# Kernel tuning notes

Hardware: AMD Instinct MI355X
Metric: run time of the kernel (lower is better)

## Reference

```python
import jax, jax.numpy as jnp
import numpy as np

NUM_GRAPHS = 128
NODES_PER_GRAPH = 512
NUM_NODES = NUM_GRAPHS * NODES_PER_GRAPH
NUM_EDGES = NUM_NODES * 16
IN_DIM = 64
HID = 128
NUM_HEADS = 4
BN_EPS = 1e-5


def setup_inputs() -> dict:
    key = jax.random.key(0)
    ks = jax.random.split(key, 12)
    x = jax.random.normal(ks[0], (NUM_NODES, IN_DIM), dtype=jnp.float32)
    edge_index = jax.random.randint(ks[1], (2, NUM_EDGES), 0, NUM_NODES, dtype=jnp.int32)
    batch = jnp.repeat(jnp.arange(NUM_GRAPHS, dtype=jnp.int32), NODES_PER_GRAPH)
    s = 0.05
    W0 = jax.random.normal(ks[2], (IN_DIM, HID), dtype=jnp.float32) * s
    b0 = jnp.zeros((HID,), jnp.float32)
    Wh = jax.random.normal(ks[3], (3, HID, HID), dtype=jnp.float32) * s  # convs 1..3
    bh = jnp.zeros((3, HID), jnp.float32)
    bn_gamma = jnp.ones((4, HID), jnp.float32)
    bn_beta = jnp.zeros((4, HID), jnp.float32)
    bn_mean = jnp.zeros((4, HID), jnp.float32)
    bn_var = jnp.ones((4, HID), jnp.float32)
    attn_in_w = jax.random.normal(ks[4], (3 * HID, HID), dtype=jnp.float32) * s
    attn_in_b = jnp.zeros((3 * HID,), jnp.float32)
    attn_out_w = jax.random.normal(ks[5], (HID, HID), dtype=jnp.float32) * s
    attn_out_b = jnp.zeros((HID,), jnp.float32)
    return dict(x=x, W0=W0, b0=b0, Wh=Wh, bh=bh, bn_gamma=bn_gamma, bn_beta=bn_beta,
                bn_mean=bn_mean, bn_var=bn_var, attn_in_w=attn_in_w, attn_in_b=attn_in_b,
                attn_out_w=attn_out_w, attn_out_b=attn_out_b, edge_index=edge_index, batch=batch)


def _forward(x, W0, b0, Wh, bh, bn_gamma, bn_beta, bn_mean, bn_var,
             attn_in_w, attn_in_b, attn_out_w, attn_out_b, edge_index, batch):
    N = x.shape[0]
    src, dst = edge_index[0], edge_index[1]
    # GCN symmetric normalization with self-loops (PyG GCNConv)
    deg = jax.ops.segment_sum(jnp.ones_like(src, jnp.float32), dst, num_segments=N) + 1.0
    dis = jax.lax.rsqrt(deg)                      # deg^{-1/2}
    enorm = (dis[src] * dis[dst])[:, None]        # per-edge norm
    self_norm = (dis * dis)[:, None]              # self-loop norm

    def gcn(h, W, b):
        h = h @ W
        agg = jax.ops.segment_sum(h[src] * enorm, dst, num_segments=N)
        return agg + h * self_norm + b

    def bn(h, i):
        scale = bn_gamma[i] * jax.lax.rsqrt(bn_var[i] + BN_EPS)
        return (h - bn_mean[i]) * scale + bn_beta[i]  # eval-mode BN

    # dropout is identity in eval mode
    h = jax.nn.relu(bn(gcn(x, W0, b0), 0))
    h = jax.nn.relu(bn(gcn(h, Wh[0], bh[0]), 1))
    h = jax.nn.relu(bn(gcn(h, Wh[1], bh[1]), 2))
    f = jax.nn.relu(bn(gcn(h, Wh[2], bh[2]), 3))   # [N, HID]

    # per-graph self-attention (equal-size contiguous graphs -> batched MHA)
    dh = HID // NUM_HEADS
    xg = f.reshape(NUM_GRAPHS, NODES_PER_GRAPH, HID)
    qkv = xg @ attn_in_w.T + attn_in_b            # [G, n, 3H]
    q, k, v = jnp.split(qkv, 3, axis=-1)

    def heads(t):
        return t.reshape(NUM_GRAPHS, NODES_PER_GRAPH, NUM_HEADS, dh).transpose(0, 2, 1, 3)
    q, k, v = heads(q), heads(k), heads(v)
    scores = jnp.einsum('ghnd,ghmd->ghnm', q, k) / np.sqrt(dh).astype(np.float32)
    attn = jax.nn.softmax(scores, axis=-1)
    o = jnp.einsum('ghnm,ghmd->ghnd', attn, v).transpose(0, 2, 1, 3).reshape(NUM_GRAPHS, NODES_PER_GRAPH, HID)
    o = o @ attn_out_w.T + attn_out_b
    final = o.reshape(N, HID)

    # global mean pool over batch indices
    cnt = jax.ops.segment_sum(jnp.ones((N,), jnp.float32), batch, num_segments=NUM_GRAPHS)
    graph_emb = jax.ops.segment_sum(final, batch, num_segments=NUM_GRAPHS) / cnt[:, None]
    return final, graph_emb


def reference(x, W0, b0, Wh, bh, bn_gamma, bn_beta, bn_mean, bn_var,
              attn_in_w, attn_in_b, attn_out_w, attn_out_b, edge_index, batch):
    return _forward(x, W0, b0, Wh, bh, bn_gamma, bn_beta, bn_mean, bn_var,
                    attn_in_w, attn_in_b, attn_out_w, attn_out_b, edge_index, batch)
```

## Files before the change

### kernel.cpp

```cpp
#include <hip/hip_runtime.h>
#include <hip/hip_bf16.h>
#include <cstdint>
#include <cstddef>

#define N_NODES 65536
#define N_EDGES 1048576
#define N_GRAPHS 128
#define NPG 512
#define IN_DIM 64
#define HID 128
#define BN_EPS 1e-5f

typedef __attribute__((ext_vector_type(8))) short bf16x8;
typedef __attribute__((ext_vector_type(4))) float f32x4;
typedef __attribute__((ext_vector_type(8))) unsigned short u16x8;

__device__ inline unsigned short f2bf(float f) {
  unsigned u = __builtin_bit_cast(unsigned, f);
  u = u + 0x7fffu + ((u >> 16) & 1u);
  return (unsigned short)(u >> 16);
}
__device__ inline float bf2f(unsigned short h) {
  unsigned u = ((unsigned)h) << 16;
  return __builtin_bit_cast(float, u);
}
__device__ inline void split_bf(float v, unsigned short& hi, unsigned short& lo) {
  hi = f2bf(v);
  lo = f2bf(v - bf2f(hi));
}
__device__ inline void split_bf_fast(float v, unsigned short& hi, unsigned short& lo) {
  unsigned u = __builtin_bit_cast(unsigned, v);
  hi = (unsigned short)(u >> 16);
  float r = v - __builtin_bit_cast(float, u & 0xffff0000u);
  lo = f2bf(r);
}

__global__ __launch_bounds__(256) void hist_kernel(const int* __restrict__ dst,
                                                   int* __restrict__ deg) {
  int e = blockIdx.x * 256 + threadIdx.x;
  if (e < N_EDGES) atomicAdd(&deg[dst[e]], 1);
}

__global__ __launch_bounds__(256) void dis_kernel(const int* __restrict__ deg,
                                                  float* __restrict__ dis) {
  int n = blockIdx.x * 256 + threadIdx.x;
  if (n < N_NODES) dis[n] = 1.0f / sqrtf((float)deg[n] + 1.0f);
}

__global__ __launch_bounds__(1024) void scan_kernel(const int* __restrict__ deg,
                                                    int* __restrict__ offsets,
                                                    int* __restrict__ cursor) {
  __shared__ int sums[1024];
  int t = threadIdx.x;
  int base = t * 64;
  const int4* dp = (const int4*)(deg + base);
  int s = 0;
#pragma unroll
  for (int i = 0; i < 16; i++) {
    int4 v = dp[i];
    s += v.x + v.y + v.z + v.w;
  }
  sums[t] = s;
  __syncthreads();
  for (int off = 1; off < 1024; off <<= 1) {
    int v = (t >= off) ? sums[t - off] : 0;
    __syncthreads();
    sums[t] += v;
    __syncthreads();
  }
  int run = (t == 0) ? 0 : sums[t - 1];
#pragma unroll
  for (int i = 0; i < 16; i++) {
    int4 v = dp[i];
    int idx = base + i * 4;
    offsets[idx] = run; cursor[idx] = run; run += v.x;
    offsets[idx + 1] = run; cursor[idx + 1] = run; run += v.y;
    offsets[idx + 2] = run; cursor[idx + 2] = run; run += v.z;
    offsets[idx + 3] = run; cursor[idx + 3] = run; run += v.w;
  }
  if (t == 1023) offsets[N_NODES] = run;
}

__global__ __launch_bounds__(256) void fill_kernel(const int* __restrict__ src,
                                                   const int* __restrict__ dst,
                                                   int* __restrict__ cursor,
                                                   int* __restrict__ csr) {
  int e = blockIdx.x * 256 + threadIdx.x;
  if (e < N_EDGES) {
    int d = dst[e];
    int slot = atomicAdd(&cursor[d], 1);
    csr[slot] = src[e];
  }
}

__global__ __launch_bounds__(256) void agg64_kernel(const float* __restrict__ x,
                                                    const float* __restrict__ dis,
                                                    const int* __restrict__ offsets,
                                                    const int* __restrict__ csr,
                                                    unsigned short* __restrict__ zhi,
                                                    unsigned short* __restrict__ zlo) {
  int node = blockIdx.x * 4 + (threadIdx.x >> 6);
  int lane = threadIdx.x & 63;
  float dn = dis[node];
  float acc = x[(size_t)node * 64 + lane] * dn * dn;
  int beg = offsets[node], end = offsets[node + 1];
  int k = beg;
  for (; k + 4 <= end; k += 4) {
    int s0 = csr[k], s1 = csr[k + 1], s2 = csr[k + 2], s3 = csr[k + 3];
    float w0 = dn * dis[s0], w1 = dn * dis[s1], w2 = dn * dis[s2], w3 = dn * dis[s3];
    float v0 = x[(size_t)s0 * 64 + lane];
    float v1 = x[(size_t)s1 * 64 + lane];
    float v2 = x[(size_t)s2 * 64 + lane];
    float v3 = x[(size_t)s3 * 64 + lane];
    acc = fmaf(w0, v0, acc);
    acc = fmaf(w1, v1, acc);
    acc = fmaf(w2, v2, acc);
    acc = fmaf(w3, v3, acc);
  }
  for (; k < end; k++) {
    int s = csr[k];
    acc = fmaf(dn * dis[s], x[(size_t)s * 64 + lane], acc);
  }
  unsigned short h_, l_;
  split_bf(acc, h_, l_);
  zhi[(size_t)node * 64 + lane] = h_;
  zlo[(size_t)node * 64 + lane] = l_;
}

__global__ __launch_bounds__(256) void agg128_kernel(const float* __restrict__ h,
                                                     const float* __restrict__ dis,
                                                     const int* __restrict__ offsets,
                                                     const int* __restrict__ csr,
                                                     unsigned short* __restrict__ zhi,
                                                     unsigned short* __restrict__ zlo) {
  int node = blockIdx.x * 4 + (threadIdx.x >> 6);
  int lane = threadIdx.x & 63;
  float dn = dis[node];
  float sn = dn * dn;
  const float* hr = h + (size_t)node * 128;
  float a0 = hr[lane] * sn;
  float a1 = hr[lane + 64] * sn;
  int beg = offsets[node], end = offsets[node + 1];
  int k = beg;
  for (; k + 4 <= end; k += 4) {
    int s0 = csr[k], s1 = csr[k + 1], s2 = csr[k + 2], s3 = csr[k + 3];
    float w0 = dn * dis[s0], w1 = dn * dis[s1], w2 = dn * dis[s2], w3 = dn * dis[s3];
    const float* p0 = h + (size_t)s0 * 128;
    const float* p1 = h + (size_t)s1 * 128;
    const float* p2 = h + (size_t)s2 * 128;
    const float* p3 = h + (size_t)s3 * 128;
    float u0 = p0[lane], d0 = p0[lane + 64];
    float u1 = p1[lane], d1 = p1[lane + 64];
    float u2 = p2[lane], d2 = p2[lane + 64];
    float u3 = p3[lane], d3 = p3[lane + 64];
    a0 = fmaf(w0, u0, a0); a1 = fmaf(w0, d0, a1);
    a0 = fmaf(w1, u1, a0); a1 = fmaf(w1, d1, a1);
    a0 = fmaf(w2, u2, a0); a1 = fmaf(w2, d2, a1);
    a0 = fmaf(w3, u3, a0); a1 = fmaf(w3, d3, a1);
  }
  for (; k < end; k++) {
    int s = csr[k];
    float w = dn * dis[s];
    const float* hs = h + (size_t)s * 128;
    a0 = fmaf(w, hs[lane], a0);
    a1 = fmaf(w, hs[lane + 64], a1);
  }
  unsigned short h0, l0, h1, l1;
  split_bf(a0, h0, l0);
  split_bf(a1, h1, l1);
  zhi[(size_t)node * 128 + lane] = h0;
  zlo[(size_t)node * 128 + lane] = l0;
  zhi[(size_t)node * 128 + lane + 64] = h1;
  zlo[(size_t)node * 128 + lane + 64] = l1;
}

template <bool TRANS>
__global__ __launch_bounds__(256) void wprep_kernel(const float* __restrict__ W, int K, int O,
                                                    unsigned short* __restrict__ hi,
                                                    unsigned short* __restrict__ lo) {
  int idx = blockIdx.x * 256 + threadIdx.x;
  int KC = K / 32;
  int total = (O / 16) * KC * 64;
  if (idx >= total) return;
  int lane = idx & 63;
  int rest = idx >> 6;
  int kc = rest % KC;
  int nt = rest / KC;
  int n = nt * 16 + (lane & 15);
  int kb = kc * 32 + (lane >> 4) * 8;
  unsigned short* hp = hi + (size_t)idx * 8;
  unsigned short* lp = lo + (size_t)idx * 8;
#pragma unroll
  for (int j = 0; j < 8; j++) {
    int k = kb + j;
    float v = TRANS ? W[(size_t)n * K + k] : W[(size_t)k * O + n];
    unsigned short h_, l_;
    split_bf(v, h_, l_);
    hp[j] = h_;
    lp[j] = l_;
  }
}

template <int K, int O, bool DOBN, bool DORELU, bool SPLIT_OUT, bool GROUPED,
          bool DOPOOL = false>
__global__ __launch_bounds__(256) void gemm_mfma(
    const unsigned short* __restrict__ Ahi, const unsigned short* __restrict__ Alo,
    const unsigned short* __restrict__ Whi, const unsigned short* __restrict__ Wlo,
    const float* __restrict__ bias,
    const float* __restrict__ gamma, const float* __restrict__ beta,
    const float* __restrict__ mean, const float* __restrict__ var,
    float* __restrict__ Cf, unsigned short* __restrict__ Chi,
    unsigned short* __restrict__ Clo, float* __restrict__ Pool = nullptr) {
  constexpr int KC = K / 32;
  int wave = threadIdx.x >> 6;
  int lane = threadIdx.x & 63;
  int m0 = blockIdx.x * 128 + wave * 32;
  int o0 = blockIdx.y * 128;
  int mrow = lane & 15;
  int kseg = (lane >> 4) * 8;

  f32x4 acc[2][8];
#pragma unroll
  for (int mt = 0; mt < 2; mt++)
#pragma unroll
    for (int nt = 0; nt < 8; nt++) acc[mt][nt] = (f32x4)0.0f;

#pragma unroll
  for (int kc = 0; kc < KC; kc++) {
    bf16x8 ah[2], al[2];
#pragma unroll
    for (int mt = 0; mt < 2; mt++) {
      size_t aoff = (size_t)(m0 + mt * 16 + mrow) * K + kc * 32 + kseg;
      ah[mt] = *(const bf16x8*)(Ahi + aoff);
      al[mt] = *(const bf16x8*)(Alo + aoff);
    }
#pragma unroll
    for (int nt = 0; nt < 8; nt++) {
      size_t foff = (((size_t)(blockIdx.y * 8 + nt) * KC + kc) * 64 + lane) * 8;
      bf16x8 bh = *(const bf16x8*)(Whi + foff);
      bf16x8 bl = *(const bf16x8*)(Wlo + foff);
#pragma unroll
      for (int mt = 0; mt < 2; mt++) {
        acc[mt][nt] = __builtin_amdgcn_mfma_f32_16x16x32_bf16(ah[mt], bh, acc[mt][nt], 0, 0, 0);
        acc[mt][nt] = __builtin_amdgcn_mfma_f32_16x16x32_bf16(ah[mt], bl, acc[mt][nt], 0, 0, 0);
        acc[mt][nt] = __builtin_amdgcn_mfma_f32_16x16x32_bf16(al[mt], bh, acc[mt][nt], 0, 0, 0);
        acc[mt][nt] = __builtin_amdgcn_mfma_f32_16x16x32_bf16(al[mt], bl, acc[mt][nt], 0, 0, 0);
      }
    }
  }

  int ccol = lane & 15;
  int crow0 = (lane >> 4) * 4;
  float colsum[8];
  if constexpr (DOPOOL) {
#pragma unroll
    for (int nt = 0; nt < 8; nt++) colsum[nt] = 0.0f;
  }
#pragma unroll
  for (int nt = 0; nt < 8; nt++) {
    int c = o0 + nt * 16 + ccol;
    float sc, cb;
    float b = bias[c];
    if (DOBN) {
      sc = gamma[c] * rsqrtf(var[c] + BN_EPS);
      cb = (b - mean[c]) * sc + beta[c];
    } else {
      sc = 1.0f;
      cb = b;
    }
#pragma unroll
    for (int mt = 0; mt < 2; mt++) {
#pragma unroll
      for (int r = 0; r < 4; r++) {
        float v = fmaf(acc[mt][nt][r], sc, cb);
        if (DORELU) v = fmaxf(v, 0.0f);
        size_t row = (size_t)(m0 + mt * 16 + crow0 + r);
        if (SPLIT_OUT) {
          unsigned short h_, l_;
          split_bf(v, h_, l_);
          if (GROUPED) {
            size_t base = row * (size_t)(2 * O) + (size_t)(((c >> 5) << 6) + (c & 31));
            Chi[base] = h_;
            Chi[base + 32] = l_;
          } else {
            Chi[row * O + c] = h_;
            Clo[row * O + c] = l_;
          }
        } else {
          Cf[row * O + c] = v;
        }
        if constexpr (DOPOOL) colsum[nt] += v;
      }
    }
  }
  if constexpr (DOPOOL) {
    __shared__ float pb[4][128];
#pragma unroll
    for (int nt = 0; nt < 8; nt++) {
      float cs = colsum[nt];
      cs += __shfl_xor(cs, 16, 64);
      cs += __shfl_xor(cs, 32, 64);
      if ((lane >> 4) == 0) pb[wave][nt * 16 + ccol] = cs;
    }
    __syncthreads();
    int tt = threadIdx.x;
    if (tt < 128) {
      float s2 = pb[0][tt] + pb[1][tt] + pb[2][tt] + pb[3][tt];
      int gg = blockIdx.x >> 2;
      atomicAdd(&Pool[gg * 128 + tt], s2 * (1.0f / NPG));
    }
  }
}

__global__ __launch_bounds__(256) void knorm_kernel(const unsigned short* __restrict__ qvs,
                                                    float* __restrict__ kmax2) {
  int g = blockIdx.x >> 2;
  int h = blockIdx.x & 3;
  size_t gbase = (size_t)g * NPG;
  float best = 0.0f;
#pragma unroll
  for (int r = 0; r < 2; r++) {
    int j = r * 256 + threadIdx.x;
    size_t base = (gbase + j) * 768 + (size_t)(4 + h) * 64;
    float s = 0.0f;
#pragma unroll
    for (int i = 0; i < 4; i++) {
      u16x8 hh = *(const u16x8*)(qvs + base + i * 8);
      u16x8 ll = *(const u16x8*)(qvs + base + 32 + i * 8);
#pragma unroll
      for (int jj = 0; jj < 8; jj++) {
        float v = bf2f(hh[jj]) + bf2f(ll[jj]);
        s = fmaf(v, v, s);
      }
    }
    best = fmaxf(best, s);
  }
#pragma unroll
  for (int off = 32; off >= 1; off >>= 1)
    best = fmaxf(best, __shfl_xor(best, off, 64));
  __shared__ float red[4];
  int wave = threadIdx.x >> 6;
  if ((threadIdx.x & 63) == 0) red[wave] = best;
  __syncthreads();
  if (threadIdx.x == 0) {
    float m = fmaxf(fmaxf(red[0], red[1]), fmaxf(red[2], red[3]));
    kmax2[blockIdx.x] = m;
  }
}

__global__ __launch_bounds__(256, 2) void attn_mfma_kernel(
    const unsigned short* __restrict__ qvs, const float* __restrict__ kmax2,
    unsigned short* __restrict__ ohi, unsigned short* __restrict__ olo) {
  int wb = ((blockIdx.x & 7) << 7) | (blockIdx.x >> 3);
  int g = wb >> 3;
  int h = (wb >> 1) & 3;
  int half = wb & 1;
  int t = threadIdx.x;
  int wave = t >> 6;
  int lane = t & 63;
  int quad = lane >> 4;
  int l15 = lane & 15;
  size_t gbase = (size_t)g * NPG;
  int qb = half * 256 + wave * 64;

  const float cf = 0.17677669529663687f * 1.4426950408889634f;

  __shared__ unsigned short Kh[2][32][40] __attribute__((aligned(16)));
  __shared__ unsigned short Kl[2][32][40] __attribute__((aligned(16)));
  __shared__ unsigned short Vh[2][33][40] __attribute__((aligned(16)));
  __shared__ unsigned short Vl[2][33][40] __attribute__((aligned(16)));
  __shared__ char wbuf[4][11264] __attribute__((aligned(16)));

  unsigned short* Ph = (unsigned short*)wbuf[wave];
  unsigned short* Pl = Ph + 64 * 44;
  float* Ot = (float*)wbuf[wave];

  bf16x8 qh[4], ql[4];
  float qn2p[4];
#pragma unroll
  for (int mt = 0; mt < 4; mt++) {
    size_t qoff = (gbase + qb + mt * 16 + l15) * 768 + (size_t)h * 64 + quad * 8;
    u16x8 hh = *(const u16x8*)(qvs + qoff);
    u16x8 ll = *(const u16x8*)(qvs + qoff + 32);
    qh[mt] = __builtin_bit_cast(bf16x8, hh);
    ql[mt] = __builtin_bit_cast(bf16x8, ll);
    float s = 0.0f;
#pragma unroll
    for (int j = 0; j < 8; j++) {
      float v = bf2f(hh[j]) + bf2f(ll[j]);
      s = fmaf(v, v, s);
    }
    s += __shfl_xor(s, 16);
    s += __shfl_xor(s, 32);
    qn2p[mt] = s;
  }
  if (quad == 0) {
#pragma unroll
    for (int mt = 0; mt < 4; mt++) Ot[mt * 16 + l15] = qn2p[mt];
  }
  float km2 = kmax2[g * 4 + h];
  float Mq[4][4];
#pragma unroll
  for (int mt = 0; mt < 4; mt++)
#pragma unroll
    for (int r = 0; r < 4; r++)
      Mq[mt][r] = cf * sqrtf(Ot[mt * 16 + quad * 4 + r] * km2);

  f32x4 Oa[4][3];
#pragma unroll
  for (int mt = 0; mt < 4; mt++)
#pragma unroll
    for (int nt = 0; nt < 3; nt++) Oa[mt][nt] = (f32x4)0.0f;

  if (t >= 64 && t < 72) {
    int u = t - 64;
    int bsel = u >> 2;
    int i = u & 3;
    u16x8 ones;
#pragma unroll
    for (int j = 0; j < 8; j++) ones[j] = 0x3F80;
    *(u16x8*)&Vh[bsel][32][i * 8] = ones;
  }

  bool isK = (t >= 128);
  bool isV = (t < 64);
  u16x8 kreg_h, kreg_l;
  ushort4 vreg_h[4], vreg_l[4];
  int kkey = 0, kds = 0, vkeyb = 0, vdvb = 0;
  if (isK) {
    int t2 = t - 128;
    kkey = t2 >> 2;
    kds = (t2 & 3) * 8;
  } else if (isV) {
    vkeyb = (t & 7) * 4;
    vdvb = (t >> 3) * 4;
  }

  auto load_chunk = [&](int c) {
    if (isK) {
      size_t ko = (gbase + (size_t)(c * 32 + kkey)) * 768 + (size_t)(4 + h) * 64 + kds;
      kreg_h = *(const u16x8*)(qvs + ko);
      kreg_l = *(const u16x8*)(qvs + ko + 32);
    } else if (isV) {
#pragma unroll
      for (int r = 0; r < 4; r++) {
        size_t vo = (gbase + (size_t)(c * 32 + vkeyb + r)) * 768 + (size_t)(8 + h) * 64 + vdvb;
        vreg_h[r] = *(const ushort4*)(qvs + vo);
        vreg_l[r] = *(const ushort4*)(qvs + vo + 32);
      }
    }
  };

  auto stage_chunk = [&](int bsel) {
    if (isK) {
      *(u16x8*)&Kh[bsel][kkey][kds] = kreg_h;
      *(u16x8*)&Kl[bsel][kkey][kds] = kreg_l;
    } else if (isV) {
      unsigned short ha[4][4], la[4][4];
#pragma unroll
      for (int r = 0; r < 4; r++) {
        *(ushort4*)&ha[r][0] = vreg_h[r];
        *(ushort4*)&la[r][0] = vreg_l[r];
      }
#pragma unroll
      for (int c2 = 0; c2 < 4; c2++) {
        ushort4 hv, lv;
        hv.x = ha[0][c2]; hv.y = ha[1][c2]; hv.z = ha[2][c2]; hv.w = ha[3][c2];
        lv.x = la[0][c2]; lv.y = la[1][c2]; lv.z = la[2][c2]; lv.w = la[3][c2];
        *(ushort4*)&Vh[bsel][vdvb + c2][vkeyb] = hv;
        *(ushort4*)&Vl[bsel][vdvb + c2][vkeyb] = lv;
      }
    }
  };

  load_chunk(0);
  stage_chunk(0);
  __syncthreads();

  int p = 0;
  for (int c = 0; c < 16; c++) {
    if (c < 15) load_chunk(c + 1);

#pragma unroll
    for (int nt = 0; nt < 2; nt++) {
      bf16x8 bkh = *(const bf16x8*)&Kh[p][nt * 16 + l15][quad * 8];
      bf16x8 bkl = *(const bf16x8*)&Kl[p][nt * 16 + l15][quad * 8];
#pragma unroll
      for (int mt = 0; mt < 4; mt++) {
        f32x4 S = (f32x4)0.0f;
        __builtin_amdgcn_s_setprio(1);
        S = __builtin_amdgcn_mfma_f32_16x16x32_bf16(qh[mt], bkh, S, 0, 0, 0);
        S = __builtin_amdgcn_mfma_f32_16x16x32_bf16(qh[mt], bkl, S, 0, 0, 0);
        S = __builtin_amdgcn_mfma_f32_16x16x32_bf16(ql[mt], bkh, S, 0, 0, 0);
        S = __builtin_amdgcn_mfma_f32_16x16x32_bf16(ql[mt], bkl, S, 0, 0, 0);
        __builtin_amdgcn_s_setprio(0);
#pragma unroll
        for (int r = 0; r < 4; r++) {
          float pexp = __builtin_exp2f(fmaf(S[r], cf, -Mq[mt][r]));
          unsigned short hi_, lo_;
          split_bf_fast(pexp, hi_, lo_);
          int row = mt * 16 + quad * 4 + r;
          Ph[row * 44 + nt * 16 + l15] = hi_;
          Pl[row * 44 + nt * 16 + l15] = lo_;
        }
      }
    }
    bf16x8 pah[4], pal[4];
#pragma unroll
    for (int mt = 0; mt < 4; mt++) {
      pah[mt] = *(const bf16x8*)&Ph[(mt * 16 + l15) * 44 + quad * 8];
      pal[mt] = *(const bf16x8*)&Pl[(mt * 16 + l15) * 44 + quad * 8];
    }
    __builtin_amdgcn_s_setprio(1);
#pragma unroll
    for (int nt = 0; nt < 3; nt++) {
      bf16x8 bvh = *(const bf16x8*)&Vh[p][nt * 16 + l15][quad * 8];
      if (nt < 2) {
        bf16x8 bvl = *(const bf16x8*)&Vl[p][nt * 16 + l15][quad * 8];
#pragma unroll
        for (int mt = 0; mt < 4; mt++) {
          Oa[mt][nt] = __builtin_amdgcn_mfma_f32_16x16x32_bf16(pah[mt], bvh, Oa[mt][nt], 0, 0, 0);
          Oa[mt][nt] = __builtin_amdgcn_mfma_f32_16x16x32_bf16(pah[mt], bvl, Oa[mt][nt], 0, 0, 0);
          Oa[mt][nt] = __builtin_amdgcn_mfma_f32_16x16x32_bf16(pal[mt], bvh, Oa[mt][nt], 0, 0, 0);
        }
      } else {
#pragma unroll
        for (int mt = 0; mt < 4; mt++) {
          Oa[mt][nt] = __builtin_amdgcn_mfma_f32_16x16x32_bf16(pah[mt], bvh, Oa[mt][nt], 0, 0, 0);
          Oa[mt][nt] = __builtin_amdgcn_mfma_f32_16x16x32_bf16(pal[mt], bvh, Oa[mt][nt], 0, 0, 0);
        }
      }
    }
    __builtin_amdgcn_s_setprio(0);

    if (c < 15) stage_chunk(p ^ 1);
    __syncthreads();
    p ^= 1;
  }

#pragma unroll
  for (int mt = 0; mt < 4; mt++) {
#pragma unroll
    for (int r = 0; r < 4; r++) {
      int row = mt * 16 + quad * 4 + r;
      Ot[row * 36 + l15] = Oa[mt][0][r];
      Ot[row * 36 + 16 + l15] = Oa[mt][1][r];
      if (l15 == 0) Ot[row * 36 + 32] = Oa[mt][2][r];
    }
  }
  {
    int row = lane;
    float inv = 1.0f / Ot[row * 36 + 32];
    size_t node = gbase + qb + row;
    u16x8 vh, vl;
#pragma unroll
    for (int seg = 0; seg < 4; seg++) {
#pragma unroll
      for (int j = 0; j < 8; j++) {
        unsigned short hi_, lo_;
        split_bf_fast(Ot[row * 36 + seg * 8 + j] * inv, hi_, lo_);
        vh[j] = hi_;
        vl[j] = lo_;
      }
      *(u16x8*)(ohi + node * 128 + h * 32 + seg * 8) = vh;
      *(u16x8*)(olo + node * 128 + h * 32 + seg * 8) = vl;
    }
  }
}

extern "C" void kernel_launch(void* const* d_in, const int* in_sizes, int n_in,
                              void* d_out, int out_size, void* d_ws, size_t ws_size,
                              hipStream_t stream) {
  (void)in_sizes; (void)n_in; (void)out_size; (void)ws_size;
  const float* x          = (const float*)d_in[0];
  const float* W0         = (const float*)d_in[1];
  const float* b0         = (const float*)d_in[2];
  const float* Wh         = (const float*)d_in[3];
  const float* bh         = (const float*)d_in[4];
  const float* bn_gamma   = (const float*)d_in[5];
  const float* bn_beta    = (const float*)d_in[6];
  const float* bn_mean    = (const float*)d_in[7];
  const float* bn_var     = (const float*)d_in[8];
  const float* attn_in_w  = (const float*)d_in[9];
  const float* attn_in_b  = (const float*)d_in[10];
  const float* attn_out_w = (const float*)d_in[11];
  const float* attn_out_b = (const float*)d_in[12];
  const int* edge_index   = (const int*)d_in[13];
  const int* src = edge_index;
  const int* dst = edge_index + N_EDGES;

  char* ws = (char*)d_ws;
  size_t off = 0;
  auto alloc = [&](size_t bytes) -> void* {
    void* p = ws + off;
    off += (bytes + 255) & ~(size_t)255;
    return p;
  };
  int*   deg     = (int*)alloc((size_t)N_NODES * 4);
  int*   offsets = (int*)alloc((size_t)(N_NODES + 1) * 4);
  int*   cursor  = (int*)alloc((size_t)N_NODES * 4);
  int*   csr     = (int*)alloc((size_t)N_EDGES * 4);
  float* dis     = (float*)alloc((size_t)N_NODES * 4);
  float* bufA    = (float*)alloc((size_t)N_NODES * HID * 4);
  unsigned short* zhi = (unsigned short*)alloc((size_t)N_NODES * HID * 2);
  unsigned short* zlo = (unsigned short*)alloc((size_t)N_NODES * HID * 2);
  unsigned short* qvs = (unsigned short*)alloc((size_t)N_NODES * 768 * 2);
  float* kmax2   = (float*)alloc((size_t)N_GRAPHS * 4 * 4);
  unsigned short* w0h = (unsigned short*)alloc(8192 * 2);
  unsigned short* w0l = (unsigned short*)alloc(8192 * 2);
  unsigned short* whh[3], *whl[3];
  for (int i = 0; i < 3; i++) {
    whh[i] = (unsigned short*)alloc(16384 * 2);
    whl[i] = (unsigned short*)alloc(16384 * 2);
  }
  unsigned short* wqh = (unsigned short*)alloc(49152 * 2);
  unsigned short* wql = (unsigned short*)alloc(49152 * 2);
  unsigned short* woh = (unsigned short*)alloc(16384 * 2);
  unsigned short* wol = (unsigned short*)alloc(16384 * 2);

  unsigned short* fhi = (unsigned short*)bufA;
  unsigned short* flo = fhi + (size_t)N_NODES * HID;

  float* fin = (float*)d_out;
  float* emb = fin + (size_t)N_NODES * HID;

  hipMemsetAsync(deg, 0, (size_t)N_NODES * 4, stream);
  hipMemsetAsync(emb, 0, (size_t)N_GRAPHS * HID * 4, stream);
  hist_kernel<<<N_EDGES / 256, 256, 0, stream>>>(dst, deg);
  dis_kernel<<<N_NODES / 256, 256, 0, stream>>>(deg, dis);
  scan_kernel<<<1, 1024, 0, stream>>>(deg, offsets, cursor);
  fill_kernel<<<N_EDGES / 256, 256, 0, stream>>>(src, dst, cursor, csr);

  wprep_kernel<false><<<4, 256, 0, stream>>>(W0, 64, 128, w0h, w0l);
  for (int i = 0; i < 3; i++)
    wprep_kernel<false><<<8, 256, 0, stream>>>(Wh + (size_t)i * HID * HID, 128, 128,
                                               whh[i], whl[i]);
  wprep_kernel<true><<<24, 256, 0, stream>>>(attn_in_w, 128, 384, wqh, wql);
  wprep_kernel<true><<<8, 256, 0, stream>>>(attn_out_w, 128, 128, woh, wol);

  dim3 ggrid(N_NODES / 128, 1);
  agg64_kernel<<<N_NODES / 4, 256, 0, stream>>>(x, dis, offsets, csr, zhi, zlo);
  gemm_mfma<64, 128, true, true, false, false><<<ggrid, 256, 0, stream>>>(
      zhi, zlo, w0h, w0l, b0, bn_gamma, bn_beta, bn_mean, bn_var, bufA, nullptr, nullptr);
  for (int L = 0; L < 2; L++) {
    agg128_kernel<<<N_NODES / 4, 256, 0, stream>>>(bufA, dis, offsets, csr, zhi, zlo);
    gemm_mfma<128, 128, true, true, false, false><<<ggrid, 256, 0, stream>>>(
        zhi, zlo, whh[L], whl[L], bh + (size_t)L * HID,
        bn_gamma + (size_t)(L + 1) * HID, bn_beta + (size_t)(L + 1) * HID,
        bn_mean + (size_t)(L + 1) * HID, bn_var + (size_t)(L + 1) * HID,
        bufA, nullptr, nullptr);
  }
  agg128_kernel<<<N_NODES / 4, 256, 0, stream>>>(bufA, dis, offsets, csr, zhi, zlo);
  gemm_mfma<128, 128, true, true, true, false><<<ggrid, 256, 0, stream>>>(
      zhi, zlo, whh[2], whl[2], bh + (size_t)2 * HID,
      bn_gamma + (size_t)3 * HID, bn_beta + (size_t)3 * HID,
      bn_mean + (size_t)3 * HID, bn_var + (size_t)3 * HID,
      nullptr, fhi, flo);
  dim3 qgrid(N_NODES / 128, 3);
  gemm_mfma<128, 384, false, false, true, true><<<qgrid, 256, 0, stream>>>(
      fhi, flo, wqh, wql, attn_in_b, nullptr, nullptr, nullptr, nullptr,
      nullptr, qvs, nullptr);
  knorm_kernel<<<N_GRAPHS * 4, 256, 0, stream>>>(qvs, kmax2);
  attn_mfma_kernel<<<N_GRAPHS * 4 * 2, 256, 0, stream>>>(qvs, kmax2, zhi, zlo);
  gemm_mfma<128, 128, false, false, false, false, true><<<ggrid, 256, 0, stream>>>(
      zhi, zlo, woh, wol, attn_out_b, nullptr, nullptr, nullptr, nullptr,
      fin, nullptr, nullptr, emb);
}
```

Baseline: 848.4 us.

## Keep attention probabilities in registers via transposed QK^T and permuted key rows

```diff
diff --git a/kernel.cpp b/kernel.cpp
--- a/kernel.cpp
+++ b/kernel.cpp
@@ -14,6 +14,7 @@
 typedef __attribute__((ext_vector_type(8))) short bf16x8;
 typedef __attribute__((ext_vector_type(4))) float f32x4;
 typedef __attribute__((ext_vector_type(8))) unsigned short u16x8;
+typedef __attribute__((ext_vector_type(4))) unsigned int u32x4;
 
 __device__ inline unsigned short f2bf(float f) {
   unsigned u = __builtin_bit_cast(unsigned, f);
@@ -369,14 +370,11 @@
   __shared__ unsigned short Kl[2][32][40] __attribute__((aligned(16)));
   __shared__ unsigned short Vh[2][33][40] __attribute__((aligned(16)));
   __shared__ unsigned short Vl[2][33][40] __attribute__((aligned(16)));
-  __shared__ char wbuf[4][11264] __attribute__((aligned(16)));
-
-  unsigned short* Ph = (unsigned short*)wbuf[wave];
-  unsigned short* Pl = Ph + 64 * 44;
-  float* Ot = (float*)wbuf[wave];
+  __shared__ float Ot[64 * 36] __attribute__((aligned(16)));
 
   bf16x8 qh[4], ql[4];
-  float qn2p[4];
+  float Mq[4];
+  float km2 = kmax2[g * 4 + h];
 #pragma unroll
   for (int mt = 0; mt < 4; mt++) {
     size_t qoff = (gbase + qb + mt * 16 + l15) * 768 + (size_t)h * 64 + quad * 8;
@@ -392,19 +390,8 @@
     }
     s += __shfl_xor(s, 16);
     s += __shfl_xor(s, 32);
-    qn2p[mt] = s;
-  }
-  if (quad == 0) {
-#pragma unroll
-    for (int mt = 0; mt < 4; mt++) Ot[mt * 16 + l15] = qn2p[mt];
-  }
-  float km2 = kmax2[g * 4 + h];
-  float Mq[4][4];
-#pragma unroll
-  for (int mt = 0; mt < 4; mt++)
-#pragma unroll
-    for (int r = 0; r < 4; r++)
-      Mq[mt][r] = cf * sqrtf(Ot[mt * 16 + quad * 4 + r] * km2);
+    Mq[mt] = cf * sqrtf(s * km2);
+  }
 
   f32x4 Oa[4][3];
 #pragma unroll
@@ -426,11 +413,14 @@
   bool isV = (t < 64);
   u16x8 kreg_h, kreg_l;
   ushort4 vreg_h[4], vreg_l[4];
-  int kkey = 0, kds = 0, vkeyb = 0, vdvb = 0;
+  int kkey = 0, kds = 0, kphys = 0, vkeyb = 0, vdvb = 0;
   if (isK) {
     int t2 = t - 128;
     kkey = t2 >> 2;
     kds = (t2 & 3) * 8;
+    int nt_ = kkey >> 4, q_ = (kkey >> 2) & 3, r_ = kkey & 3;
+    int p_ = (nt_ << 1) | (r_ >> 1);
+    kphys = 8 * (q_ ^ p_) + 2 * p_ + (r_ & 1);
   } else if (isV) {
     vkeyb = (t & 7) * 4;
     vdvb = (t >> 3) * 4;
@@ -438,7 +428,7 @@
 
   auto load_chunk = [&](int c) {
     if (isK) {
-      size_t ko = (gbase + (size_t)(c * 32 + kkey)) * 768 + (size_t)(4 + h) * 64 + kds;
+      size_t ko = (gbase + (size_t)(c * 32 + kphys)) * 768 + (size_t)(4 + h) * 64 + kds;
       kreg_h = *(const u16x8*)(qvs + ko);
       kreg_l = *(const u16x8*)(qvs + ko + 32);
     } else if (isV) {
@@ -481,90 +471,94 @@
   for (int c = 0; c < 16; c++) {
     if (c < 15) load_chunk(c + 1);
 
-#pragma unroll
-    for (int nt = 0; nt < 2; nt++) {
-      bf16x8 bkh = *(const bf16x8*)&Kh[p][nt * 16 + l15][quad * 8];
-      bf16x8 bkl = *(const bf16x8*)&Kl[p][nt * 16 + l15][quad * 8];
-#pragma unroll
-      for (int mt = 0; mt < 4; mt++) {
+    bf16x8 akh[2], akl[2];
+    akh[0] = *(const bf16x8*)&Kh[p][l15][quad * 8];
+    akh[1] = *(const bf16x8*)&Kh[p][16 + l15][quad * 8];
+    akl[0] = *(const bf16x8*)&Kl[p][l15][quad * 8];
+    akl[1] = *(const bf16x8*)&Kl[p][16 + l15][quad * 8];
+    bf16x8 bvh0 = *(const bf16x8*)&Vh[p][l15][quad * 8];
+    bf16x8 bvl0 = *(const bf16x8*)&Vl[p][l15][quad * 8];
+    bf16x8 bvh1 = *(const bf16x8*)&Vh[p][16 + l15][quad * 8];
+    bf16x8 bvl1 = *(const bf16x8*)&Vl[p][16 + l15][quad * 8];
+    bf16x8 bvh2 = *(const bf16x8*)&Vh[p][32 + l15][quad * 8];
+
+#pragma unroll
+    for (int mt = 0; mt < 4; mt++) {
+      unsigned pkh[4], pkl[4];
+#pragma unroll
+      for (int nt = 0; nt < 2; nt++) {
         f32x4 S = (f32x4)0.0f;
-        __builtin_amdgcn_s_setprio(1);
-        S = __builtin_amdgcn_mfma_f32_16x16x32_bf16(qh[mt], bkh, S, 0, 0, 0);
-        S = __builtin_amdgcn_mfma_f32_16x16x32_bf16(qh[mt], bkl, S, 0, 0, 0);
-        S = __builtin_amdgcn_mfma_f32_16x16x32_bf16(ql[mt], bkh, S, 0, 0, 0);
-        S = __builtin_amdgcn_mfma_f32_16x16x32_bf16(ql[mt], bkl, S, 0, 0, 0);
-        __builtin_amdgcn_s_setprio(0);
-#pragma unroll
-        for (int r = 0; r < 4; r++) {
-          float pexp = __builtin_exp2f(fmaf(S[r], cf, -Mq[mt][r]));
-          unsigned short hi_, lo_;
-          split_bf_fast(pexp, hi_, lo_);
-          int row = mt * 16 + quad * 4 + r;
-          Ph[row * 44 + nt * 16 + l15] = hi_;
-          Pl[row * 44 + nt * 16 + l15] = lo_;
-        }
-      }
-    }
-    bf16x8 pah[4], pal[4];
-#pragma unroll
-    for (int mt = 0; mt < 4; mt++) {
-      pah[mt] = *(const bf16x8*)&Ph[(mt * 16 + l15) * 44 + quad * 8];
-      pal[mt] = *(const bf16x8*)&Pl[(mt * 16 + l15) * 44 + quad * 8];
-    }
-    __builtin_amdgcn_s_setprio(1);
-#pragma unroll
-    for (int nt = 0; nt < 3; nt++) {
-      bf16x8 bvh = *(const bf16x8*)&Vh[p][nt * 16 + l15][quad * 8];
-      if (nt < 2) {
-        bf16x8 bvl = *(const bf16x8*)&Vl[p][nt * 16 + l15][quad * 8];
-#pragma unroll
-        for (int mt = 0; mt < 4; mt++) {
-          Oa[mt][nt] = __builtin_amdgcn_mfma_f32_16x16x32_bf16(pah[mt], bvh, Oa[mt][nt], 0, 0, 0);
-          Oa[mt][nt] = __builtin_amdgcn_mfma_f32_16x16x32_bf16(pah[mt], bvl, Oa[mt][nt], 0, 0, 0);
-          Oa[mt][nt] = __builtin_amdgcn_mfma_f32_16x16x32_bf16(pal[mt], bvh, Oa[mt][nt], 0, 0, 0);
-        }
-      } else {
-#pragma unroll
-        for (int mt = 0; mt < 4; mt++) {
-          Oa[mt][nt] = __builtin_amdgcn_mfma_f32_16x16x32_bf16(pah[mt], bvh, Oa[mt][nt], 0, 0, 0);
-          Oa[mt][nt] = __builtin_amdgcn_mfma_f32_16x16x32_bf16(pal[mt], bvh, Oa[mt][nt], 0, 0, 0);
-        }
-      }
-    }
-    __builtin_amdgcn_s_setprio(0);
+        S = __builtin_amdgcn_mfma_f32_16x16x32_bf16(akh[nt], qh[mt], S, 0, 0, 0);
+        S = __builtin_amdgcn_mfma_f32_16x16x32_bf16(akh[nt], ql[mt], S, 0, 0, 0);
+        S = __builtin_amdgcn_mfma_f32_16x16x32_bf16(akl[nt], qh[mt], S, 0, 0, 0);
+        S = __builtin_amdgcn_mfma_f32_16x16x32_bf16(akl[nt], ql[mt], S, 0, 0, 0);
+        unsigned short h0, l0, h1, l1, h2, l2, h3, l3;
+        split_bf_fast(__builtin_exp2f(fmaf(S[0], cf, -Mq[mt])), h0, l0);
+        split_bf_fast(__builtin_exp2f(fmaf(S[1], cf, -Mq[mt])), h1, l1);
+        split_bf_fast(__builtin_exp2f(fmaf(S[2], cf, -Mq[mt])), h2, l2);
+        split_bf_fast(__builtin_exp2f(fmaf(S[3], cf, -Mq[mt])), h3, l3);
+        pkh[nt * 2]     = (unsigned)h0 | ((unsigned)h1 << 16);
+        pkh[nt * 2 + 1] = (unsigned)h2 | ((unsigned)h3 << 16);
+        pkl[nt * 2]     = (unsigned)l0 | ((unsigned)l1 << 16);
+        pkl[nt * 2 + 1] = (unsigned)l2 | ((unsigned)l3 << 16);
+      }
+      u32x4 uh, ul;
+      uh[0] = pkh[0];
+      uh[1] = (unsigned)__shfl_xor((int)pkh[1], 16, 64);
+      uh[2] = (unsigned)__shfl_xor((int)pkh[2], 32, 64);
+      uh[3] = (unsigned)__shfl_xor((int)pkh[3], 48, 64);
+      ul[0] = pkl[0];
+      ul[1] = (unsigned)__shfl_xor((int)pkl[1], 16, 64);
+      ul[2] = (unsigned)__shfl_xor((int)pkl[2], 32, 64);
+      ul[3] = (unsigned)__shfl_xor((int)pkl[3], 48, 64);
+      bf16x8 pa_h = __builtin_bit_cast(bf16x8, uh);
+      bf16x8 pa_l = __builtin_bit_cast(bf16x8, ul);
+
+      Oa[mt][0] = __builtin_amdgcn_mfma_f32_16x16x32_bf16(pa_h, bvh0, Oa[mt][0], 0, 0, 0);
+      Oa[mt][0] = __builtin_amdgcn_mfma_f32_16x16x32_bf16(pa_h, bvl0, Oa[mt][0], 0, 0, 0);
+      Oa[mt][0] = __builtin_amdgcn_mfma_f32_16x16x32_bf16(pa_l, bvh0, Oa[mt][0], 0, 0, 0);
+      Oa[mt][1] = __builtin_amdgcn_mfma_f32_16x16x32_bf16(pa_h, bvh1, Oa[mt][1], 0, 0, 0);
+      Oa[mt][1] = __builtin_amdgcn_mfma_f32_16x16x32_bf16(pa_h, bvl1, Oa[mt][1], 0, 0, 0);
+      Oa[mt][1] = __builtin_amdgcn_mfma_f32_16x16x32_bf16(pa_l, bvh1, Oa[mt][1], 0, 0, 0);
+      Oa[mt][2] = __builtin_amdgcn_mfma_f32_16x16x32_bf16(pa_h, bvh2, Oa[mt][2], 0, 0, 0);
+      Oa[mt][2] = __builtin_amdgcn_mfma_f32_16x16x32_bf16(pa_l, bvh2, Oa[mt][2], 0, 0, 0);
+    }
 
     if (c < 15) stage_chunk(p ^ 1);
     __syncthreads();
     p ^= 1;
   }
 
-#pragma unroll
-  for (int mt = 0; mt < 4; mt++) {
-#pragma unroll
-    for (int r = 0; r < 4; r++) {
-      int row = mt * 16 + quad * 4 + r;
-      Ot[row * 36 + l15] = Oa[mt][0][r];
-      Ot[row * 36 + 16 + l15] = Oa[mt][1][r];
-      if (l15 == 0) Ot[row * 36 + 32] = Oa[mt][2][r];
-    }
-  }
-  {
-    int row = lane;
-    float inv = 1.0f / Ot[row * 36 + 32];
-    size_t node = gbase + qb + row;
-    u16x8 vh, vl;
-#pragma unroll
-    for (int seg = 0; seg < 4; seg++) {
-#pragma unroll
-      for (int j = 0; j < 8; j++) {
-        unsigned short hi_, lo_;
-        split_bf_fast(Ot[row * 36 + seg * 8 + j] * inv, hi_, lo_);
-        vh[j] = hi_;
-        vl[j] = lo_;
-      }
-      *(u16x8*)(ohi + node * 128 + h * 32 + seg * 8) = vh;
-      *(u16x8*)(olo + node * 128 + h * 32 + seg * 8) = vl;
-    }
+  for (int w = 0; w < 4; w++) {
+    if (wave == w) {
+#pragma unroll
+      for (int mt = 0; mt < 4; mt++) {
+#pragma unroll
+        for (int r = 0; r < 4; r++) {
+          int row = mt * 16 + quad * 4 + r;
+          Ot[row * 36 + l15] = Oa[mt][0][r];
+          Ot[row * 36 + 16 + l15] = Oa[mt][1][r];
+          if (l15 == 0) Ot[row * 36 + 32] = Oa[mt][2][r];
+        }
+      }
+      int row = lane;
+      float inv = 1.0f / Ot[row * 36 + 32];
+      size_t node = gbase + qb + row;
+      u16x8 vh, vl;
+#pragma unroll
+      for (int seg = 0; seg < 4; seg++) {
+#pragma unroll
+        for (int j = 0; j < 8; j++) {
+          unsigned short hi_, lo_;
+          split_bf_fast(Ot[row * 36 + seg * 8 + j] * inv, hi_, lo_);
+          vh[j] = hi_;
+          vl[j] = lo_;
+        }
+        *(u16x8*)(ohi + node * 128 + h * 32 + seg * 8) = vh;
+        *(u16x8*)(olo + node * 128 + h * 32 + seg * 8) = vl;
+      }
+    }
+    __syncthreads();
   }
 }
 
```

Measured after the change: 806.2 us. -5.0%, faster.
